# Performance work log

Hardware: AMD Instinct MI355X
Metric: run time of the kernel (lower is better)

## Reference

```python
import math
import jax, jax.numpy as jnp
import numpy as np

NUM_FREQ = 10  # NeRF-style L=10 -> enc dim 3 + 3*2*10 = 63

def pos_encode(coords):
    # freq_bands = 2^i * pi, i = 0..L-1
    freq = (2.0 ** jnp.arange(NUM_FREQ, dtype=coords.dtype)) * math.pi
    scaled = coords[..., None] * freq                      # [E, 3, L]
    enc = jnp.stack([jnp.sin(scaled), jnp.cos(scaled)], axis=-1)  # [E, 3, L, 2]
    enc = enc.reshape(coords.shape[0], -1)                 # [E, 60] interleaved sin/cos
    return jnp.concatenate([coords, enc], axis=-1)         # [E, 63]

def setup_inputs() -> dict:
    key = jax.random.key(0)
    ks = jax.random.split(key, 9)
    N, M, K, C = 65536, 16384, 32, 64
    E = M * K
    x = jax.random.normal(ks[0], (N, C), jnp.float32)
    pos = jax.random.normal(ks[1], (N, 3), jnp.float32)
    batch = jnp.sort(jax.random.randint(ks[2], (N,), 0, 8))
    idx = jax.random.randint(ks[3], (M,), 0, N)
    row = jnp.sort(jax.random.randint(ks[4], (E,), 0, M))
    col = jax.random.randint(ks[5], (E,), 0, N)
    d_in = C + 3 + 3 * 2 * NUM_FREQ  # 127
    def lin(k, i, o):
        s = 1.0 / np.sqrt(i)
        kw, kb = jax.random.split(k)
        return (jax.random.uniform(kw, (i, o), jnp.float32, -s, s),
                jax.random.uniform(kb, (o,), jnp.float32, -s, s))
    lw1, lb1 = lin(ks[6], d_in, 128)
    lw2, lb2 = lin(ks[7], 128, 128)
    gw, gb = lin(ks[8], 128, 256)
    return dict(x=x, pos=pos, batch=batch, idx=idx, row=row, col=col,
                lw1=lw1, lb1=lb1, lw2=lw2, lb2=lb2, gw=gw, gb=gb)

def reference(x, pos, batch, idx, row, col, lw1, lb1, lw2, lb2, gw, gb):
    M = idx.shape[0]
    pos_idx = pos[idx]                         # [M, 3] sampled centers
    pos_diff = pos[col] - pos_idx[row]         # [E, 3] neighbor offsets
    pe = pos_encode(pos_diff)                  # [E, 63]
    edge_in = jnp.concatenate([x[col], pe], axis=-1)   # [E, 127]
    # local_nn: Linear->ReLU->Linear (no final activation, per MLP_Wrapper)
    h = jax.nn.relu(edge_in @ lw1 + lb1)       # [E, 128]
    edge_feat = h @ lw2 + lb2                  # [E, 128]
    # scatter_reduce amax, include_self=False: empty rows stay 0
    agg = jax.ops.segment_max(edge_feat, row, num_segments=M)
    agg = jnp.where(jnp.isneginf(agg), jnp.zeros((), agg.dtype), agg)
    out = agg @ gw + gb                        # [M, 256] global_nn (single Linear)
    return out, pos_idx, batch[idx]
```

## Files before the change

kernel.cpp:

```cpp
#include <hip/hip_runtime.h>
#include <math.h>

#define NN 65536
#define MM 16384
#define EE 524288
#define CF 64
#define HD 128
#define OD 256
#define RPB 16
#define PITCH 129

typedef __bf16 bf16x8 __attribute__((ext_vector_type(8)));
typedef __bf16 bf16x4 __attribute__((ext_vector_type(4)));
typedef float f32x4 __attribute__((ext_vector_type(4)));

__device__ __forceinline__ unsigned enc_f(float f) {
    unsigned u = __float_as_uint(f);
    return (u & 0x80000000u) ? ~u : (u | 0x80000000u);
}
__device__ __forceinline__ float dec_f(unsigned e) {
    unsigned u = (e & 0x80000000u) ? (e ^ 0x80000000u) : ~e;
    return __uint_as_float(u);
}
#define ENC_NEG_INF 0x007FFFFFu

__device__ __forceinline__ unsigned bf_bits(float f) {
    __bf16 b = (__bf16)f;
    return (unsigned)__builtin_bit_cast(unsigned short, b);
}

#define WS_FRAG_OFF 0
#define WS_ROWPTR_OFF 65536

__global__ void k_pre(__bf16* __restrict__ fragbuf, int* __restrict__ rowptr,
                      const float* __restrict__ lw1, const float* __restrict__ lw2,
                      const int* __restrict__ row,
                      const float* __restrict__ pos, const int* __restrict__ batch,
                      const int* __restrict__ idx, float* __restrict__ out) {
    const int b = blockIdx.x;
    const int t = threadIdx.x;
    if (b == 0) {
        const int lane = t & 63;
        const int wv = t >> 6;
        const int q = lane >> 4;
        const int ln = lane & 15;
        #pragma unroll
        for (int fi = 0; fi < 16; ++fi) {
            const int nt = (fi >> 2) & 1, kk = fi & 3;
            const int n = wv * 32 + nt * 16 + ln;
            bf16x8 f;
            #pragma unroll
            for (int j = 0; j < 8; ++j) {
                const int c = kk * 32 + q * 8 + j;
                const int rk = (c < 67) ? c : c - 1;
                f[j] = (fi < 8) ? (__bf16)((c == 67) ? 0.0f : lw1[rk * HD + n])
                                : (__bf16)lw2[c * HD + n];
            }
            *(bf16x8*)&fragbuf[((size_t)fi * 256 + t) * 8] = f;
        }
    } else if (b <= 65) {
        const int i = (b - 1) * 256 + t;
        if (i <= MM) {
            int lo = 0, hi = EE;
            while (lo < hi) { int mid = (lo + hi) >> 1; if (row[mid] < i) lo = mid + 1; else hi = mid; }
            rowptr[i] = lo;
        }
    } else {
        const int m = (b - 66) * 256 + t;
        if (m < MM) {
            const int s = idx[m];
            out[MM * OD + m * 3 + 0] = pos[s * 3 + 0];
            out[MM * OD + m * 3 + 1] = pos[s * 3 + 1];
            out[MM * OD + m * 3 + 2] = pos[s * 3 + 2];
            out[MM * OD + MM * 3 + m] = (float)batch[s];
        }
    }
}

__launch_bounds__(256)
__global__ void k_fused(const float* __restrict__ x, const float* __restrict__ pos,
                        const int* __restrict__ idx, const int* __restrict__ row,
                        const int* __restrict__ col, const int* __restrict__ rowptr,
                        const __bf16* __restrict__ fragbuf,
                        const float* __restrict__ lb1, const float* __restrict__ lb2,
                        const float* __restrict__ gw, const float* __restrict__ gb,
                        float* __restrict__ out) {
    __shared__ __align__(16) __bf16 einX[2][64][64];
    __shared__ __align__(16) __bf16 einP[64][64];
    __shared__ __align__(16) __bf16 hbuf[64][HD];
    __shared__ unsigned maxbuf[(RPB + 1) * PITCH];
    __shared__ int srow[2][64];
    const int t = threadIdx.x;
    const int lane = t & 63;
    const int wv = t >> 6;
    const int q = lane >> 4;
    const int ln = lane & 15;
    const int lsw = ln & 7;
    const int m0 = blockIdx.x * RPB;

    const int es = rowptr[m0];
    const int ee = rowptr[m0 + RPB];
    const int ntiles = (ee - es + 63) >> 6;

    for (int i = t; i < (RPB + 1) * PITCH; i += 256) maxbuf[i] = ENC_NEG_INF;

    const int pe_e = t >> 2, pe_part = t & 3, pe_esw = pe_e & 7;
    float4 v0, v1, v2, v3;
    auto issue = [&](int tt) {
        const int eg = min(es + tt * 64 + pe_e, EE - 1);
        const int c = col[eg];
        const float4* xr = (const float4*)(x + (size_t)c * CF) + pe_part * 4;
        v0 = xr[0]; v1 = xr[1]; v2 = xr[2]; v3 = xr[3];
    };
    auto commit = [&](int b) {
        bf16x8 pk;
        pk[0] = (__bf16)v0.x; pk[1] = (__bf16)v0.y; pk[2] = (__bf16)v0.z; pk[3] = (__bf16)v0.w;
        pk[4] = (__bf16)v1.x; pk[5] = (__bf16)v1.y; pk[6] = (__bf16)v1.z; pk[7] = (__bf16)v1.w;
        *(bf16x8*)&einX[b][pe_e][((pe_part * 2 + 0) ^ pe_esw) * 8] = pk;
        pk[0] = (__bf16)v2.x; pk[1] = (__bf16)v2.y; pk[2] = (__bf16)v2.z; pk[3] = (__bf16)v2.w;
        pk[4] = (__bf16)v3.x; pk[5] = (__bf16)v3.y; pk[6] = (__bf16)v3.z; pk[7] = (__bf16)v3.w;
        *(bf16x8*)&einX[b][pe_e][((pe_part * 2 + 1) ^ pe_esw) * 8] = pk;
    };
    auto do_pe = [&](int tt) {
        if (t < 192) {
            const int e = t & 63, d = t >> 6;
            const int sb = tt & 1;
            const int eidx = es + tt * 64 + e;
            const int eg = min(eidx, EE - 1);
            const int r = row[eg];
            const int c = col[eg];
            const int s = idx[r];
            const int esw = e & 7;
            const float pd = pos[c * 3 + d] - pos[s * 3 + d];
            if (d == 0) {
                srow[sb][e] = (eidx < ee) ? (r - m0) : RPB;
                const float pd1 = pos[c * 3 + 1] - pos[s * 3 + 1];
                const float pd2 = pos[c * 3 + 2] - pos[s * 3 + 2];
                uint2 pkt;
                pkt.x = bf_bits(pd) | (bf_bits(pd1) << 16);
                pkt.y = bf_bits(pd2);
                *(uint2*)&einP[e][esw * 8] = pkt;
            }
            const float fr = __builtin_amdgcn_fractf(pd * 0.5f);
            float sv = __builtin_amdgcn_sinf(fr);
            float cv = __builtin_amdgcn_cosf(fr);
            #pragma unroll
            for (int l = 0; l < 10; ++l) {
                const int jP = 4 + d * 20 + l * 2;
                *(unsigned*)&einP[e][((jP >> 3) ^ esw) * 8 + (jP & 7)] =
                    bf_bits(sv) | (bf_bits(cv) << 16);
                const float s2 = 2.0f * sv * cv;
                const float c2 = 1.0f - 2.0f * sv * sv;
                sv = s2; cv = c2;
            }
        }
    };

    if (ntiles > 0) issue(0);

    bf16x8 w1f[2][4];
    #pragma unroll
    for (int nt = 0; nt < 2; ++nt)
        #pragma unroll
        for (int kk = 0; kk < 4; ++kk)
            w1f[nt][kk] = *(const bf16x8*)&fragbuf[((size_t)(nt * 4 + kk) * 256 + t) * 8];
    float4 b1q[2];
    #pragma unroll
    for (int nt = 0; nt < 2; ++nt)
        b1q[nt] = *(const float4*)&lb1[wv * 32 + nt * 16 + q * 4];

    if (ntiles > 0) {
        commit(0);
        do_pe(0);
        if (ntiles > 1) issue(1);
    }
    __syncthreads();

    for (int tt = 0; tt < ntiles; ++tt) {
        const int p = tt & 1;

        f32x4 acc[2][4];
        #pragma unroll
        for (int nt = 0; nt < 2; ++nt)
            #pragma unroll
            for (int et = 0; et < 4; ++et)
                acc[nt][et] = (f32x4){b1q[nt].x, b1q[nt].y, b1q[nt].z, b1q[nt].w};
        #pragma unroll
        for (int et = 0; et < 4; ++et) {
            const int e = et * 16 + ln;
            bf16x8 a[4];
            a[0] = *(const bf16x8*)&einX[p][e][(q ^ lsw) * 8];
            a[1] = *(const bf16x8*)&einX[p][e][((4 + q) ^ lsw) * 8];
            a[2] = *(const bf16x8*)&einP[e][(q ^ lsw) * 8];
            a[3] = *(const bf16x8*)&einP[e][((4 + q) ^ lsw) * 8];
            #pragma unroll
            for (int kk = 0; kk < 4; ++kk) {
                acc[0][et] = __builtin_amdgcn_mfma_f32_16x16x32_bf16(w1f[0][kk], a[kk], acc[0][et], 0, 0, 0);
                acc[1][et] = __builtin_amdgcn_mfma_f32_16x16x32_bf16(w1f[1][kk], a[kk], acc[1][et], 0, 0, 0);
            }
        }
        if (tt + 1 < ntiles) commit(p ^ 1);
        if (tt + 2 < ntiles) issue(tt + 2);
        #pragma unroll
        for (int et = 0; et < 4; ++et) {
            const int e = et * 16 + ln;
            #pragma unroll
            for (int nt = 0; nt < 2; ++nt) {
                bf16x4 hv;
                hv[0] = (__bf16)fmaxf(acc[nt][et][0], 0.0f);
                hv[1] = (__bf16)fmaxf(acc[nt][et][1], 0.0f);
                hv[2] = (__bf16)fmaxf(acc[nt][et][2], 0.0f);
                hv[3] = (__bf16)fmaxf(acc[nt][et][3], 0.0f);
                const int chunk = wv * 4 + nt * 2 + (q >> 1);
                *(bf16x4*)&hbuf[e][((chunk ^ lsw) * 8) + (q & 1) * 4] = hv;
            }
        }
        __syncthreads();

        {
            bf16x8 w2f[2][4];
            #pragma unroll
            for (int nt = 0; nt < 2; ++nt)
                #pragma unroll
                for (int kk = 0; kk < 4; ++kk)
                    w2f[nt][kk] = *(const bf16x8*)&fragbuf[((size_t)(8 + nt * 4 + kk) * 256 + t) * 8];

            f32x4 acc2[4][2];
            #pragma unroll
            for (int nt = 0; nt < 2; ++nt) {
                const float b2 = lb2[wv * 32 + nt * 16 + ln];
                #pragma unroll
                for (int et = 0; et < 4; ++et)
                    acc2[et][nt] = (f32x4){b2, b2, b2, b2};
            }
            #pragma unroll
            for (int et = 0; et < 4; ++et) {
                const int e = et * 16 + ln;
                #pragma unroll
                for (int kk = 0; kk < 4; ++kk) {
                    bf16x8 ah = *(const bf16x8*)&hbuf[e][((kk * 4 + q) ^ lsw) * 8];
                    acc2[et][0] = __builtin_amdgcn_mfma_f32_16x16x32_bf16(ah, w2f[0][kk], acc2[et][0], 0, 0, 0);
                    acc2[et][1] = __builtin_amdgcn_mfma_f32_16x16x32_bf16(ah, w2f[1][kk], acc2[et][1], 0, 0, 0);
                }
            }
            if (tt + 1 < ntiles) do_pe(tt + 1);
            const int sb = tt & 1;
            #pragma unroll
            for (int et = 0; et < 4; ++et) {
                const int4 R = *(const int4*)&srow[sb][et * 16 + q * 4];
                #pragma unroll
                for (int nt = 0; nt < 2; ++nt) {
                    unsigned* base = maxbuf + (wv * 32 + nt * 16 + ln);
                    const f32x4 vv = acc2[et][nt];
                    int cur = R.x;
                    float m = vv[0];
                    if (R.y != cur) { atomicMax(base + cur * PITCH, enc_f(m)); cur = R.y; m = vv[1]; }
                    else m = fmaxf(m, vv[1]);
                    if (R.z != cur) { atomicMax(base + cur * PITCH, enc_f(m)); cur = R.z; m = vv[2]; }
                    else m = fmaxf(m, vv[2]);
                    if (R.w != cur) { atomicMax(base + cur * PITCH, enc_f(m)); cur = R.w; m = vv[3]; }
                    else m = fmaxf(m, vv[3]);
                    atomicMax(base + cur * PITCH, enc_f(m));
                }
            }
        }
        __syncthreads();
    }

    float* afin = (float*)hbuf;
    for (int i = t; i < RPB * HD; i += 256) {
        const unsigned e = maxbuf[(i >> 7) * PITCH + (i & 127)];
        afin[i] = (e == ENC_NEG_INF) ? 0.0f : dec_f(e);
    }
    __syncthreads();

    const int j4 = (t & 63) * 4;
    const int rbase = (t >> 6) * 4;
    float facc[4][4];
    const float4 bias = *(const float4*)&gb[j4];
    #pragma unroll
    for (int r = 0; r < 4; ++r) { facc[r][0] = bias.x; facc[r][1] = bias.y; facc[r][2] = bias.z; facc[r][3] = bias.w; }
    for (int k = 0; k < 128; k += 4) {
        float4 w0 = *(const float4*)&gw[(k + 0) * OD + j4];
        float4 w1 = *(const float4*)&gw[(k + 1) * OD + j4];
        float4 w2 = *(const float4*)&gw[(k + 2) * OD + j4];
        float4 w3 = *(const float4*)&gw[(k + 3) * OD + j4];
        #pragma unroll
        for (int r = 0; r < 4; ++r) {
            float4 av = *(const float4*)&afin[(rbase + r) * HD + k];
            facc[r][0] += av.x * w0.x + av.y * w1.x + av.z * w2.x + av.w * w3.x;
            facc[r][1] += av.x * w0.y + av.y * w1.y + av.z * w2.y + av.w * w3.y;
            facc[r][2] += av.x * w0.z + av.y * w1.z + av.z * w2.z + av.w * w3.z;
            facc[r][3] += av.x * w0.w + av.y * w1.w + av.z * w2.w + av.w * w3.w;
        }
    }
    #pragma unroll
    for (int r = 0; r < 4; ++r) {
        float4 v; v.x = facc[r][0]; v.y = facc[r][1]; v.z = facc[r][2]; v.w = facc[r][3];
        *(float4*)&out[(size_t)(m0 + rbase + r) * OD + j4] = v;
    }
}

extern "C" void kernel_launch(void* const* d_in, const int* in_sizes, int n_in,
                              void* d_out, int out_size, void* d_ws, size_t ws_size,
                              hipStream_t stream) {
    const float* x   = (const float*)d_in[0];
    const float* pos = (const float*)d_in[1];
    const int* batch = (const int*)d_in[2];
    const int* idx   = (const int*)d_in[3];
    const int* row   = (const int*)d_in[4];
    const int* col   = (const int*)d_in[5];
    const float* lw1 = (const float*)d_in[6];
    const float* lb1 = (const float*)d_in[7];
    const float* lw2 = (const float*)d_in[8];
    const float* lb2 = (const float*)d_in[9];
    const float* gw  = (const float*)d_in[10];
    const float* gb  = (const float*)d_in[11];
    float* out = (float*)d_out;
    __bf16* fragbuf = (__bf16*)((char*)d_ws + WS_FRAG_OFF);
    int* rowptr     = (int*)((char*)d_ws + WS_ROWPTR_OFF);

    hipLaunchKernelGGL(k_pre, dim3(1 + 65 + 64), dim3(256), 0, stream,
                       fragbuf, rowptr, lw1, lw2, row, pos, batch, idx, out);
    hipLaunchKernelGGL(k_fused, dim3(MM / RPB), dim3(256), 0, stream,
                       x, pos, idx, row, col, rowptr, fragbuf, lb1, lb2, gw, gb, out);
}
```

Measured before the change: 102.5 us.

## Precompute bf16 features and per-edge position offsets in pre-kernel

The pre-kernel gains two new block ranges. One converts x to a bf16 copy in workspace; the other computes each edge's pos[col] - pos[idx[row]] into a float4 buffer. The fused kernel then gathers bf16 rows, half the bytes of fp32, and reads one float4 per edge instead of the dependent row→idx→pos chain. The X staging buffer becomes single-buffered, with the commit moved after the layer-1 barrier, which frees shared memory but shortens the prefetch overlap. The cost is an extra full pass over x plus an 8 MB offset buffer written and read back.

```diff
diff --git a/kernel.cpp b/kernel.cpp
--- a/kernel.cpp
+++ b/kernel.cpp
@@ -31,10 +31,14 @@
 
 #define WS_FRAG_OFF 0
 #define WS_ROWPTR_OFF 65536
+#define WS_XBF_OFF 131072
+#define WS_PD_OFF (131072 + 8388608)
 
 __global__ void k_pre(__bf16* __restrict__ fragbuf, int* __restrict__ rowptr,
+                      __bf16* __restrict__ xbf, float4* __restrict__ pdbuf,
                       const float* __restrict__ lw1, const float* __restrict__ lw2,
-                      const int* __restrict__ row,
+                      const float* __restrict__ x, const int* __restrict__ row,
+                      const int* __restrict__ col,
                       const float* __restrict__ pos, const int* __restrict__ batch,
                       const int* __restrict__ idx, float* __restrict__ out) {
     const int b = blockIdx.x;
@@ -65,7 +69,7 @@
             while (lo < hi) { int mid = (lo + hi) >> 1; if (row[mid] < i) lo = mid + 1; else hi = mid; }
             rowptr[i] = lo;
         }
-    } else {
+    } else if (b <= 129) {
         const int m = (b - 66) * 256 + t;
         if (m < MM) {
             const int s = idx[m];
@@ -74,18 +78,39 @@
             out[MM * OD + m * 3 + 2] = pos[s * 3 + 2];
             out[MM * OD + MM * 3 + m] = (float)batch[s];
         }
+    } else if (b <= 1153) {
+        const size_t base = ((size_t)(b - 130) * 256 + t) * 16;
+        const float4* xs = (const float4*)(x + base);
+        const float4 a = xs[0], c = xs[1], d = xs[2], e = xs[3];
+        bf16x8 o0, o1;
+        o0[0] = (__bf16)a.x; o0[1] = (__bf16)a.y; o0[2] = (__bf16)a.z; o0[3] = (__bf16)a.w;
+        o0[4] = (__bf16)c.x; o0[5] = (__bf16)c.y; o0[6] = (__bf16)c.z; o0[7] = (__bf16)c.w;
+        o1[0] = (__bf16)d.x; o1[1] = (__bf16)d.y; o1[2] = (__bf16)d.z; o1[3] = (__bf16)d.w;
+        o1[4] = (__bf16)e.x; o1[5] = (__bf16)e.y; o1[6] = (__bf16)e.z; o1[7] = (__bf16)e.w;
+        *(bf16x8*)&xbf[base] = o0;
+        *(bf16x8*)&xbf[base + 8] = o1;
+    } else {
+        const int e = (b - 1154) * 256 + t;
+        const int r = row[e];
+        const int c = col[e];
+        const int s = idx[r];
+        float4 pd;
+        pd.x = pos[c * 3 + 0] - pos[s * 3 + 0];
+        pd.y = pos[c * 3 + 1] - pos[s * 3 + 1];
+        pd.z = pos[c * 3 + 2] - pos[s * 3 + 2];
+        pd.w = 0.0f;
+        pdbuf[e] = pd;
     }
 }
 
 __launch_bounds__(256)
-__global__ void k_fused(const float* __restrict__ x, const float* __restrict__ pos,
-                        const int* __restrict__ idx, const int* __restrict__ row,
-                        const int* __restrict__ col, const int* __restrict__ rowptr,
-                        const __bf16* __restrict__ fragbuf,
+__global__ void k_fused(const __bf16* __restrict__ xbf, const float4* __restrict__ pdbuf,
+                        const int* __restrict__ row, const int* __restrict__ col,
+                        const int* __restrict__ rowptr, const __bf16* __restrict__ fragbuf,
                         const float* __restrict__ lb1, const float* __restrict__ lb2,
                         const float* __restrict__ gw, const float* __restrict__ gb,
                         float* __restrict__ out) {
-    __shared__ __align__(16) __bf16 einX[2][64][64];
+    __shared__ __align__(16) __bf16 einX[64][64];
     __shared__ __align__(16) __bf16 einP[64][64];
     __shared__ __align__(16) __bf16 hbuf[64][HD];
     __shared__ unsigned maxbuf[(RPB + 1) * PITCH];
@@ -105,21 +130,16 @@
     for (int i = t; i < (RPB + 1) * PITCH; i += 256) maxbuf[i] = ENC_NEG_INF;
 
     const int pe_e = t >> 2, pe_part = t & 3, pe_esw = pe_e & 7;
-    float4 v0, v1, v2, v3;
+    bf16x8 s0, s1;
     auto issue = [&](int tt) {
         const int eg = min(es + tt * 64 + pe_e, EE - 1);
         const int c = col[eg];
-        const float4* xr = (const float4*)(x + (size_t)c * CF) + pe_part * 4;
-        v0 = xr[0]; v1 = xr[1]; v2 = xr[2]; v3 = xr[3];
+        const bf16x8* xr = (const bf16x8*)(xbf + (size_t)c * CF) + pe_part * 2;
+        s0 = xr[0]; s1 = xr[1];
     };
-    auto commit = [&](int b) {
-        bf16x8 pk;
-        pk[0] = (__bf16)v0.x; pk[1] = (__bf16)v0.y; pk[2] = (__bf16)v0.z; pk[3] = (__bf16)v0.w;
-        pk[4] = (__bf16)v1.x; pk[5] = (__bf16)v1.y; pk[6] = (__bf16)v1.z; pk[7] = (__bf16)v1.w;
-        *(bf16x8*)&einX[b][pe_e][((pe_part * 2 + 0) ^ pe_esw) * 8] = pk;
-        pk[0] = (__bf16)v2.x; pk[1] = (__bf16)v2.y; pk[2] = (__bf16)v2.z; pk[3] = (__bf16)v2.w;
-        pk[4] = (__bf16)v3.x; pk[5] = (__bf16)v3.y; pk[6] = (__bf16)v3.z; pk[7] = (__bf16)v3.w;
-        *(bf16x8*)&einX[b][pe_e][((pe_part * 2 + 1) ^ pe_esw) * 8] = pk;
+    auto commit = [&]() {
+        *(bf16x8*)&einX[pe_e][((pe_part * 2 + 0) ^ pe_esw) * 8] = s0;
+        *(bf16x8*)&einX[pe_e][((pe_part * 2 + 1) ^ pe_esw) * 8] = s1;
     };
     auto do_pe = [&](int tt) {
         if (t < 192) {
@@ -127,18 +147,14 @@
             const int sb = tt & 1;
             const int eidx = es + tt * 64 + e;
             const int eg = min(eidx, EE - 1);
-            const int r = row[eg];
-            const int c = col[eg];
-            const int s = idx[r];
             const int esw = e & 7;
-            const float pd = pos[c * 3 + d] - pos[s * 3 + d];
+            const float4 P = pdbuf[eg];
+            const float pd = (d == 0) ? P.x : ((d == 1) ? P.y : P.z);
             if (d == 0) {
-                srow[sb][e] = (eidx < ee) ? (r - m0) : RPB;
-                const float pd1 = pos[c * 3 + 1] - pos[s * 3 + 1];
-                const float pd2 = pos[c * 3 + 2] - pos[s * 3 + 2];
+                srow[sb][e] = (eidx < ee) ? (row[eg] - m0) : RPB;
                 uint2 pkt;
-                pkt.x = bf_bits(pd) | (bf_bits(pd1) << 16);
-                pkt.y = bf_bits(pd2);
+                pkt.x = bf_bits(P.x) | (bf_bits(P.y) << 16);
+                pkt.y = bf_bits(P.z);
                 *(uint2*)&einP[e][esw * 8] = pkt;
             }
             const float fr = __builtin_amdgcn_fractf(pd * 0.5f);
@@ -156,8 +172,6 @@
         }
     };
 
-    if (ntiles > 0) issue(0);
-
     bf16x8 w1f[2][4];
     #pragma unroll
     for (int nt = 0; nt < 2; ++nt)
@@ -170,15 +184,14 @@
         b1q[nt] = *(const float4*)&lb1[wv * 32 + nt * 16 + q * 4];
 
     if (ntiles > 0) {
-        commit(0);
+        issue(0);
+        commit();
         do_pe(0);
         if (ntiles > 1) issue(1);
     }
     __syncthreads();
 
     for (int tt = 0; tt < ntiles; ++tt) {
-        const int p = tt & 1;
-
         f32x4 acc[2][4];
         #pragma unroll
         for (int nt = 0; nt < 2; ++nt)
@@ -189,8 +202,8 @@
         for (int et = 0; et < 4; ++et) {
             const int e = et * 16 + ln;
             bf16x8 a[4];
-            a[0] = *(const bf16x8*)&einX[p][e][(q ^ lsw) * 8];
-            a[1] = *(const bf16x8*)&einX[p][e][((4 + q) ^ lsw) * 8];
+            a[0] = *(const bf16x8*)&einX[e][(q ^ lsw) * 8];
+            a[1] = *(const bf16x8*)&einX[e][((4 + q) ^ lsw) * 8];
             a[2] = *(const bf16x8*)&einP[e][(q ^ lsw) * 8];
             a[3] = *(const bf16x8*)&einP[e][((4 + q) ^ lsw) * 8];
             #pragma unroll
@@ -199,8 +212,6 @@
                 acc[1][et] = __builtin_amdgcn_mfma_f32_16x16x32_bf16(w1f[1][kk], a[kk], acc[1][et], 0, 0, 0);
             }
         }
-        if (tt + 1 < ntiles) commit(p ^ 1);
-        if (tt + 2 < ntiles) issue(tt + 2);
         #pragma unroll
         for (int et = 0; et < 4; ++et) {
             const int e = et * 16 + ln;
@@ -218,6 +229,7 @@
         __syncthreads();
 
         {
+            if (tt + 1 < ntiles) { commit(); issue(tt + 2 < ntiles ? tt + 2 : tt + 1); }
             bf16x8 w2f[2][4];
             #pragma unroll
             for (int nt = 0; nt < 2; ++nt)
@@ -319,9 +331,11 @@
     float* out = (float*)d_out;
     __bf16* fragbuf = (__bf16*)((char*)d_ws + WS_FRAG_OFF);
     int* rowptr     = (int*)((char*)d_ws + WS_ROWPTR_OFF);
-
-    hipLaunchKernelGGL(k_pre, dim3(1 + 65 + 64), dim3(256), 0, stream,
-                       fragbuf, rowptr, lw1, lw2, row, pos, batch, idx, out);
+    __bf16* xbf     = (__bf16*)((char*)d_ws + WS_XBF_OFF);
+    float4* pdbuf   = (float4*)((char*)d_ws + WS_PD_OFF);
+
+    hipLaunchKernelGGL(k_pre, dim3(1 + 65 + 64 + 1024 + 2048), dim3(256), 0, stream,
+                       fragbuf, rowptr, xbf, pdbuf, lw1, lw2, x, row, col, pos, batch, idx, out);
     hipLaunchKernelGGL(k_fused, dim3(MM / RPB), dim3(256), 0, stream,
-                       x, pos, idx, row, col, rowptr, fragbuf, lb1, lb2, gw, gb, out);
-}
+                       xbf, pdbuf, row, col, rowptr, fragbuf, lb1, lb2, gw, gb, out);
+}
```

Result: faster. 99.77 us (-2.7%).
